# Optimization experiments

Hardware: AMD Instinct MI355X
Metric: run time of the kernel (lower is better)

Reference implementation:

```python
import jax, jax.numpy as jnp
import numpy as np

IN_FEATS = 128
HIDDEN = 32
OUT_CLASSES = 2
N_NODES = 100000
N_EDGES = 625000


def setup_inputs() -> dict:
    key = jax.random.key(0)
    k1, k2, k3, k4, k5, k6, k7 = jax.random.split(key, 7)
    src_nodes = jax.random.randint(k1, (N_EDGES,), 0, N_NODES, dtype=jnp.int64 if jax.config.jax_enable_x64 else jnp.int32)
    dst_nodes = jax.random.randint(k2, (N_EDGES,), 0, N_NODES, dtype=jnp.int64 if jax.config.jax_enable_x64 else jnp.int32)
    node_embed = jax.random.normal(k3, (N_NODES, IN_FEATS), dtype=jnp.float32)
    # Linear params (torch nn.Linear default init: U(-1/sqrt(fan_in), 1/sqrt(fan_in)))
    lim1 = 1.0 / np.sqrt(2 * IN_FEATS)
    W1 = jax.random.uniform(k4, (HIDDEN, 2 * IN_FEATS), jnp.float32, -lim1, lim1)
    b1 = jax.random.uniform(k5, (HIDDEN,), jnp.float32, -lim1, lim1)
    lim2 = 1.0 / np.sqrt(HIDDEN)
    W2 = jax.random.uniform(k6, (OUT_CLASSES, HIDDEN), jnp.float32, -lim2, lim2)
    b2 = jax.random.uniform(k7, (OUT_CLASSES,), jnp.float32, -lim2, lim2)
    return {"src_nodes": src_nodes, "dst_nodes": dst_nodes, "node_embed": node_embed,
            "W1": W1, "b1": b1, "W2": W2, "b2": b2}


def reference(src_nodes, dst_nodes, node_embed, W1, b1, W2, b2):
    # Gather endpoint embeddings: [E, F] each
    src_e = node_embed[src_nodes]
    dst_e = node_embed[dst_nodes]
    # Avoid materializing the concat explicitly in the GEMM by splitting W1:
    # fc1(cat([s, d])) == s @ W1[:, :F].T + d @ W1[:, F:].T + b1
    W1s, W1d = W1[:, :IN_FEATS], W1[:, IN_FEATS:]
    h = jax.nn.relu(src_e @ W1s.T + dst_e @ W1d.T + b1)  # [E, 32]
    logits = h @ W2.T + b2  # [E, out_classes]
    return logits
```

## Files before the change

### kernel.cpp

```cpp
#include <hip/hip_runtime.h>

#define IN_FEATS 128
#define HIDDEN 32

typedef short v8s __attribute__((ext_vector_type(8)));
typedef unsigned short u16x8 __attribute__((ext_vector_type(8)));
typedef float v4f __attribute__((ext_vector_type(4)));

__device__ __forceinline__ unsigned short f2bf(float x) {
    union { float f; unsigned int u; } v; v.f = x;
    const unsigned int r = v.u + 0x7fffu + ((v.u >> 16) & 1u);
    return (unsigned short)(r >> 16);
}
__device__ __forceinline__ float bf2f(unsigned short b) {
    union { float f; unsigned int u; } v; v.u = ((unsigned int)b) << 16;
    return v.f;
}

__global__ __launch_bounds__(256) void pack_W_frags(
    const float* __restrict__ W1,
    unsigned short* __restrict__ Bhi,
    unsigned short* __restrict__ Blo)
{
    const int i = blockIdx.x * 256 + threadIdx.x;
    if (i >= 4 * 4 * 64 * 8) return;
    const int j    = i & 7;
    const int lane = (i >> 3) & 63;
    const int ks   = (i >> 9) & 3;
    const int nb   = i >> 11;
    const int u = nb * 16 + (lane & 15);
    const int k = ks * 32 + ((lane >> 4) & 3) * 8 + j;
    const float w = W1[(u & 31) * (2 * IN_FEATS) + (u >> 5) * IN_FEATS + k];
    const unsigned short hi = f2bf(w);
    Bhi[i] = hi;
    Blo[i] = f2bf(w - bf2f(hi));
}

__global__ __launch_bounds__(256, 4) void precompute_P_mfma(
    const float* __restrict__ embed,
    const unsigned short* __restrict__ Bhi,
    const unsigned short* __restrict__ Blo,
    unsigned short* __restrict__ P,
    int n_nodes)
{
    const int t    = threadIdx.x;
    const int lane = t & 63;
    const int wave = t >> 6;
    const int node0 = blockIdx.x * 64 + wave * 16;
    if (node0 >= n_nodes) return;
    const int last = n_nodes - 1;
    const int row  = min(node0 + (lane & 15), last);
    const int grp  = lane >> 4;

    v8s ahi[4], alo[4];
#pragma unroll
    for (int ks = 0; ks < 4; ++ks) {
        const float* ap = embed + (size_t)row * IN_FEATS + ks * 32 + grp * 8;
        const float4 x0 = *reinterpret_cast<const float4*>(ap);
        const float4 x1 = *reinterpret_cast<const float4*>(ap + 4);
        const float xs[8] = {x0.x, x0.y, x0.z, x0.w, x1.x, x1.y, x1.z, x1.w};
        v8s h, l;
#pragma unroll
        for (int j = 0; j < 8; ++j) {
            const unsigned short hb = f2bf(xs[j]);
            h[j] = (short)hb;
            l[j] = (short)f2bf(xs[j] - bf2f(hb));
        }
        ahi[ks] = h;
        alo[ks] = l;
    }

#pragma unroll
    for (int nb = 0; nb < 4; ++nb) {
        v8s bhi[4], blo[4];
#pragma unroll
        for (int ks = 0; ks < 4; ++ks) {
            const int fi = ((nb * 4 + ks) * 64 + lane) * 8;
            bhi[ks] = *reinterpret_cast<const v8s*>(Bhi + fi);
            blo[ks] = *reinterpret_cast<const v8s*>(Blo + fi);
        }
        v4f acc = {0.f, 0.f, 0.f, 0.f};
#pragma unroll
        for (int ks = 0; ks < 4; ++ks) {
            acc = __builtin_amdgcn_mfma_f32_16x16x32_bf16(ahi[ks], bhi[ks], acc, 0, 0, 0);
            acc = __builtin_amdgcn_mfma_f32_16x16x32_bf16(ahi[ks], blo[ks], acc, 0, 0, 0);
            acc = __builtin_amdgcn_mfma_f32_16x16x32_bf16(alo[ks], bhi[ks], acc, 0, 0, 0);
        }
        const int u = nb * 16 + (lane & 15);
#pragma unroll
        for (int r = 0; r < 4; ++r) {
            const int n = node0 + grp * 4 + r;
            if (n < n_nodes)
                P[(size_t)n * 64 + u] = f2bf(acc[r]);
        }
    }
}

__global__ __launch_bounds__(256) void edge_classify_bf16(
    const int* __restrict__ src,
    const int* __restrict__ dst,
    const unsigned short* __restrict__ P,
    const float* __restrict__ b1,
    const float* __restrict__ W2,
    const float* __restrict__ b2,
    float* __restrict__ out,
    int n_edges)
{
    const int t = threadIdx.x;
    const int e = blockIdx.x * 64 + (t >> 2);
    if (e >= n_edges) return;
    const int q = t & 3;
    const int s = src[e];
    const int d = dst[e];

    const u16x8 ps = *reinterpret_cast<const u16x8*>(P + (size_t)s * 64 + q * 8);
    const u16x8 pd = *reinterpret_cast<const u16x8*>(P + (size_t)d * 64 + 32 + q * 8);

    const float4 b1a = *reinterpret_cast<const float4*>(b1 + q * 8);
    const float4 b1b = *reinterpret_cast<const float4*>(b1 + q * 8 + 4);
    const float4 w0a = *reinterpret_cast<const float4*>(W2 + q * 8);
    const float4 w0b = *reinterpret_cast<const float4*>(W2 + q * 8 + 4);
    const float4 w1a = *reinterpret_cast<const float4*>(W2 + HIDDEN + q * 8);
    const float4 w1b = *reinterpret_cast<const float4*>(W2 + HIDDEN + q * 8 + 4);
    const float bb1[8] = {b1a.x, b1a.y, b1a.z, b1a.w, b1b.x, b1b.y, b1b.z, b1b.w};
    const float ww0[8] = {w0a.x, w0a.y, w0a.z, w0a.w, w0b.x, w0b.y, w0b.z, w0b.w};
    const float ww1[8] = {w1a.x, w1a.y, w1a.z, w1a.w, w1b.x, w1b.y, w1b.z, w1b.w};

    float l0 = 0.f, l1 = 0.f;
#pragma unroll
    for (int j = 0; j < 8; ++j) {
        float h = bf2f(ps[j]) + bf2f(pd[j]) + bb1[j];
        h = fmaxf(h, 0.f);
        l0 = fmaf(h, ww0[j], l0);
        l1 = fmaf(h, ww1[j], l1);
    }
    l0 += __shfl_xor(l0, 1);
    l0 += __shfl_xor(l0, 2);
    l1 += __shfl_xor(l1, 1);
    l1 += __shfl_xor(l1, 2);
    if (q == 0)
        *reinterpret_cast<float2*>(out + (size_t)e * 2) =
            make_float2(l0 + b2[0], l1 + b2[1]);
}

__global__ __launch_bounds__(256) void edge_direct(
    const int* __restrict__ src, const int* __restrict__ dst,
    const float* __restrict__ embed,
    const float* __restrict__ W1, const float* __restrict__ b1,
    const float* __restrict__ W2, const float* __restrict__ b2,
    float* __restrict__ out, int n_edges)
{
    const int e = blockIdx.x * 256 + threadIdx.x;
    if (e >= n_edges) return;
    const int s = src[e], d = dst[e];
    const float* se = embed + (size_t)s * IN_FEATS;
    const float* de = embed + (size_t)d * IN_FEATS;

    float acc[HIDDEN];
#pragma unroll
    for (int hh = 0; hh < HIDDEN; ++hh) acc[hh] = b1[hh];

    for (int c = 0; c < 4; ++c) {
        float es[32], ed[32];
#pragma unroll
        for (int q = 0; q < 8; ++q) {
            const float4 v = *reinterpret_cast<const float4*>(se + c * 32 + q * 4);
            es[q*4+0] = v.x; es[q*4+1] = v.y; es[q*4+2] = v.z; es[q*4+3] = v.w;
            const float4 u = *reinterpret_cast<const float4*>(de + c * 32 + q * 4);
            ed[q*4+0] = u.x; ed[q*4+1] = u.y; ed[q*4+2] = u.z; ed[q*4+3] = u.w;
        }
#pragma unroll
        for (int hh = 0; hh < HIDDEN; ++hh) {
            float acch = acc[hh];
#pragma unroll
            for (int k = 0; k < 32; ++k) {
                acch = fmaf(es[k], W1[hh * 256 + c * 32 + k], acch);
                acch = fmaf(ed[k], W1[hh * 256 + 128 + c * 32 + k], acch);
            }
            acc[hh] = acch;
        }
    }

    float l0 = b2[0], l1 = b2[1];
#pragma unroll
    for (int hh = 0; hh < HIDDEN; ++hh) {
        const float hv = fmaxf(acc[hh], 0.f);
        l0 = fmaf(hv, W2[hh], l0);
        l1 = fmaf(hv, W2[HIDDEN + hh], l1);
    }
    *reinterpret_cast<float2*>(out + (size_t)e * 2) = make_float2(l0, l1);
}

extern "C" void kernel_launch(void* const* d_in, const int* in_sizes, int n_in,
                              void* d_out, int out_size, void* d_ws, size_t ws_size,
                              hipStream_t stream)
{
    const int*   src = (const int*)d_in[0];
    const int*   dst = (const int*)d_in[1];
    const float* emb = (const float*)d_in[2];
    const float* W1  = (const float*)d_in[3];
    const float* b1  = (const float*)d_in[4];
    const float* W2  = (const float*)d_in[5];
    const float* b2  = (const float*)d_in[6];
    float* out = (float*)d_out;

    const int n_edges = in_sizes[0];
    const int n_nodes = in_sizes[2] / IN_FEATS;

    const size_t p_bytes = (size_t)n_nodes * 64 * sizeof(unsigned short);
    const size_t b_elems = 4 * 4 * 64 * 8;
    const size_t need = p_bytes + 2 * b_elems * sizeof(unsigned short);

    if (ws_size >= need && (p_bytes & 15) == 0) {
        unsigned short* P   = (unsigned short*)d_ws;
        unsigned short* Bhi = (unsigned short*)((char*)d_ws + p_bytes);
        unsigned short* Blo = Bhi + b_elems;
        pack_W_frags<<<(int)((b_elems + 255) / 256), 256, 0, stream>>>(W1, Bhi, Blo);
        const int nb_nodes = (n_nodes + 63) / 64;
        precompute_P_mfma<<<nb_nodes, 256, 0, stream>>>(emb, Bhi, Blo, P, n_nodes);
        const int nb_edges4 = (n_edges + 63) / 64;
        edge_classify_bf16<<<nb_edges4, 256, 0, stream>>>(src, dst, P, b1, W2, b2, out, n_edges);
    } else {
        const int nb_edges = (n_edges + 255) / 256;
        edge_direct<<<nb_edges, 256, 0, stream>>>(src, dst, emb, W1, b1, W2, b2, out, n_edges);
    }
}
```

Before: 46.53 us.

## Fuse weight packing, node projection and edge classification into one cooperative kernel

Replaces the three-kernel pipeline (pack W1 fragments, per-node MFMA projection, per-edge gather/classify) with a single persistent cooperative kernel. Each block packs the W1 bf16 hi/lo fragments into shared memory, grid-strides over 16-node tiles to write P, then crosses a grid-wide barrier and grid-strides over edges, two edges per quad per iteration. This is meant to remove two kernel launches and the global round trip of the packed weights, and to add memory-level parallelism in the gather phase. In exchange it adds a grid sync, redundant weight packing in every block, per-call host device-property and occupancy queries, and 32 KB of LDS per block that may limit occupancy.

```diff
diff --git a/kernel.cpp b/kernel.cpp
--- a/kernel.cpp
+++ b/kernel.cpp
@@ -1,4 +1,7 @@
 #include <hip/hip_runtime.h>
+#include <hip/hip_cooperative_groups.h>
+
+namespace cg = cooperative_groups;
 
 #define IN_FEATS 128
 #define HIDDEN 32
@@ -15,6 +18,159 @@
 __device__ __forceinline__ float bf2f(unsigned short b) {
     union { float f; unsigned int u; } v; v.u = ((unsigned int)b) << 16;
     return v.f;
+}
+
+__global__ __launch_bounds__(256, 4) void fused_edge_classifier(
+    const float* __restrict__ embed,
+    const float* __restrict__ W1,
+    const float* __restrict__ b1,
+    const float* __restrict__ W2,
+    const float* __restrict__ b2,
+    const int* __restrict__ src,
+    const int* __restrict__ dst,
+    unsigned short* __restrict__ P,
+    float* __restrict__ out,
+    int n_nodes,
+    int n_edges)
+{
+    __shared__ unsigned short sBhi[8192];
+    __shared__ unsigned short sBlo[8192];
+
+    const int t    = threadIdx.x;
+    const int lane = t & 63;
+    const int wave = t >> 6;
+
+#pragma unroll
+    for (int g0 = 0; g0 < 1024; g0 += 256) {
+        const int g   = g0 + t;
+        const int gl  = g & 63;
+        const int ks  = (g >> 6) & 3;
+        const int nb  = g >> 8;
+        const int u   = nb * 16 + (gl & 15);
+        const int k0  = ks * 32 + ((gl >> 4) & 3) * 8;
+        const float* wp = W1 + (u & 31) * (2 * IN_FEATS) + (u >> 5) * IN_FEATS + k0;
+        const float4 x0 = *reinterpret_cast<const float4*>(wp);
+        const float4 x1 = *reinterpret_cast<const float4*>(wp + 4);
+        const float xs[8] = {x0.x, x0.y, x0.z, x0.w, x1.x, x1.y, x1.z, x1.w};
+        v8s h, l;
+#pragma unroll
+        for (int j = 0; j < 8; ++j) {
+            const unsigned short hb = f2bf(xs[j]);
+            h[j] = (short)hb;
+            l[j] = (short)f2bf(xs[j] - bf2f(hb));
+        }
+        *reinterpret_cast<v8s*>(sBhi + g * 8) = h;
+        *reinterpret_cast<v8s*>(sBlo + g * 8) = l;
+    }
+    __syncthreads();
+
+    const int last = n_nodes - 1;
+    const int grp  = lane >> 4;
+    const int gwid = blockIdx.x * 4 + wave;
+    const int nw   = gridDim.x * 4;
+    const int ntiles = (n_nodes + 15) >> 4;
+
+    for (int tile = gwid; tile < ntiles; tile += nw) {
+        const int node0 = tile << 4;
+        const int row   = min(node0 + (lane & 15), last);
+
+        v8s ahi[4], alo[4];
+#pragma unroll
+        for (int ks = 0; ks < 4; ++ks) {
+            const float* ap = embed + (size_t)row * IN_FEATS + ks * 32 + grp * 8;
+            const float4 x0 = *reinterpret_cast<const float4*>(ap);
+            const float4 x1 = *reinterpret_cast<const float4*>(ap + 4);
+            const float xs[8] = {x0.x, x0.y, x0.z, x0.w, x1.x, x1.y, x1.z, x1.w};
+            v8s h, l;
+#pragma unroll
+            for (int j = 0; j < 8; ++j) {
+                const unsigned short hb = f2bf(xs[j]);
+                h[j] = (short)hb;
+                l[j] = (short)f2bf(xs[j] - bf2f(hb));
+            }
+            ahi[ks] = h;
+            alo[ks] = l;
+        }
+
+#pragma unroll
+        for (int nb = 0; nb < 4; ++nb) {
+            v8s bhi[4], blo[4];
+#pragma unroll
+            for (int ks = 0; ks < 4; ++ks) {
+                const int fi = ((nb * 4 + ks) * 64 + lane) * 8;
+                bhi[ks] = *reinterpret_cast<const v8s*>(sBhi + fi);
+                blo[ks] = *reinterpret_cast<const v8s*>(sBlo + fi);
+            }
+            v4f acc = {0.f, 0.f, 0.f, 0.f};
+#pragma unroll
+            for (int ks = 0; ks < 4; ++ks) {
+                acc = __builtin_amdgcn_mfma_f32_16x16x32_bf16(ahi[ks], bhi[ks], acc, 0, 0, 0);
+                acc = __builtin_amdgcn_mfma_f32_16x16x32_bf16(ahi[ks], blo[ks], acc, 0, 0, 0);
+                acc = __builtin_amdgcn_mfma_f32_16x16x32_bf16(alo[ks], bhi[ks], acc, 0, 0, 0);
+            }
+            const int u = nb * 16 + (lane & 15);
+#pragma unroll
+            for (int r = 0; r < 4; ++r) {
+                const int n = node0 + grp * 4 + r;
+                if (n < n_nodes)
+                    P[(size_t)n * 64 + u] = f2bf(acc[r]);
+            }
+        }
+    }
+
+    cg::this_grid().sync();
+
+    const int q = t & 3;
+    const float4 b1a = *reinterpret_cast<const float4*>(b1 + q * 8);
+    const float4 b1b = *reinterpret_cast<const float4*>(b1 + q * 8 + 4);
+    const float4 w0a = *reinterpret_cast<const float4*>(W2 + q * 8);
+    const float4 w0b = *reinterpret_cast<const float4*>(W2 + q * 8 + 4);
+    const float4 w1a = *reinterpret_cast<const float4*>(W2 + HIDDEN + q * 8);
+    const float4 w1b = *reinterpret_cast<const float4*>(W2 + HIDDEN + q * 8 + 4);
+    const float bb1[8] = {b1a.x, b1a.y, b1a.z, b1a.w, b1b.x, b1b.y, b1b.z, b1b.w};
+    const float ww0[8] = {w0a.x, w0a.y, w0a.z, w0a.w, w0b.x, w0b.y, w0b.z, w0b.w};
+    const float ww1[8] = {w1a.x, w1a.y, w1a.z, w1a.w, w1b.x, w1b.y, w1b.z, w1b.w};
+    const float bias0 = b2[0], bias1 = b2[1];
+
+    const int qid0 = (blockIdx.x * 256 + t) >> 2;
+    const int nq   = gridDim.x * 64;
+
+    for (int e = qid0; e < n_edges; e += 2 * nq) {
+        const int eBr = e + nq;
+        const bool hasB = eBr < n_edges;
+        const int eB = hasB ? eBr : e;
+
+        const int s1 = src[e],  d1 = dst[e];
+        const int s2 = src[eB], d2 = dst[eB];
+        const u16x8 ps1 = *reinterpret_cast<const u16x8*>(P + (size_t)s1 * 64 + q * 8);
+        const u16x8 pd1 = *reinterpret_cast<const u16x8*>(P + (size_t)d1 * 64 + 32 + q * 8);
+        const u16x8 ps2 = *reinterpret_cast<const u16x8*>(P + (size_t)s2 * 64 + q * 8);
+        const u16x8 pd2 = *reinterpret_cast<const u16x8*>(P + (size_t)d2 * 64 + 32 + q * 8);
+
+        float a0 = 0.f, a1 = 0.f, c0 = 0.f, c1 = 0.f;
+#pragma unroll
+        for (int j = 0; j < 8; ++j) {
+            float h1 = bf2f(ps1[j]) + bf2f(pd1[j]) + bb1[j];
+            float h2 = bf2f(ps2[j]) + bf2f(pd2[j]) + bb1[j];
+            h1 = fmaxf(h1, 0.f);
+            h2 = fmaxf(h2, 0.f);
+            a0 = fmaf(h1, ww0[j], a0);
+            a1 = fmaf(h1, ww1[j], a1);
+            c0 = fmaf(h2, ww0[j], c0);
+            c1 = fmaf(h2, ww1[j], c1);
+        }
+        a0 += __shfl_xor(a0, 1); a0 += __shfl_xor(a0, 2);
+        a1 += __shfl_xor(a1, 1); a1 += __shfl_xor(a1, 2);
+        c0 += __shfl_xor(c0, 1); c0 += __shfl_xor(c0, 2);
+        c1 += __shfl_xor(c1, 1); c1 += __shfl_xor(c1, 2);
+        if (q == 0) {
+            *reinterpret_cast<float2*>(out + (size_t)e * 2) =
+                make_float2(a0 + bias0, a1 + bias1);
+            if (hasB)
+                *reinterpret_cast<float2*>(out + (size_t)eBr * 2) =
+                    make_float2(c0 + bias0, c1 + bias1);
+        }
+    }
 }
 
 __global__ __launch_bounds__(256) void pack_W_frags(
@@ -134,10 +290,8 @@
         l0 = fmaf(h, ww0[j], l0);
         l1 = fmaf(h, ww1[j], l1);
     }
-    l0 += __shfl_xor(l0, 1);
-    l0 += __shfl_xor(l0, 2);
-    l1 += __shfl_xor(l1, 1);
-    l1 += __shfl_xor(l1, 2);
+    l0 += __shfl_xor(l0, 1); l0 += __shfl_xor(l0, 2);
+    l1 += __shfl_xor(l1, 1); l1 += __shfl_xor(l1, 2);
     if (q == 0)
         *reinterpret_cast<float2*>(out + (size_t)e * 2) =
             make_float2(l0 + b2[0], l1 + b2[1]);
@@ -209,19 +363,44 @@
 
     const size_t p_bytes = (size_t)n_nodes * 64 * sizeof(unsigned short);
     const size_t b_elems = 4 * 4 * 64 * 8;
-    const size_t need = p_bytes + 2 * b_elems * sizeof(unsigned short);
-
-    if (ws_size >= need && (p_bytes & 15) == 0) {
-        unsigned short* P   = (unsigned short*)d_ws;
-        unsigned short* Bhi = (unsigned short*)((char*)d_ws + p_bytes);
-        unsigned short* Blo = Bhi + b_elems;
-        pack_W_frags<<<(int)((b_elems + 255) / 256), 256, 0, stream>>>(W1, Bhi, Blo);
-        const int nb_nodes = (n_nodes + 63) / 64;
-        precompute_P_mfma<<<nb_nodes, 256, 0, stream>>>(emb, Bhi, Blo, P, n_nodes);
-        const int nb_edges4 = (n_edges + 63) / 64;
-        edge_classify_bf16<<<nb_edges4, 256, 0, stream>>>(src, dst, P, b1, W2, b2, out, n_edges);
-    } else {
+
+    if (ws_size < p_bytes + 2 * b_elems * sizeof(unsigned short)) {
         const int nb_edges = (n_edges + 255) / 256;
         edge_direct<<<nb_edges, 256, 0, stream>>>(src, dst, emb, W1, b1, W2, b2, out, n_edges);
-    }
-}
+        return;
+    }
+
+    unsigned short* P = (unsigned short*)d_ws;
+
+    int dev = 0;
+    (void)hipGetDevice(&dev);
+    hipDeviceProp_t prop;
+    int coop_ok = (hipGetDeviceProperties(&prop, dev) == hipSuccess) &&
+                  prop.cooperativeLaunch;
+    int blocks_per_cu = 0;
+    if (coop_ok) {
+        coop_ok = (hipOccupancyMaxActiveBlocksPerMultiprocessor(
+                       &blocks_per_cu, (const void*)fused_edge_classifier,
+                       256, 0) == hipSuccess) && blocks_per_cu > 0;
+    }
+    if (coop_ok) {
+        const int grid = blocks_per_cu * prop.multiProcessorCount;
+        void* args[] = {
+            (void*)&emb, (void*)&W1, (void*)&b1, (void*)&W2, (void*)&b2,
+            (void*)&src, (void*)&dst, (void*)&P, (void*)&out,
+            (void*)&n_nodes, (void*)&n_edges
+        };
+        if (hipLaunchCooperativeKernel((const void*)fused_edge_classifier,
+                                       dim3(grid), dim3(256), args, 0,
+                                       stream) == hipSuccess)
+            return;
+    }
+
+    unsigned short* Bhi = (unsigned short*)((char*)d_ws + p_bytes);
+    unsigned short* Blo = Bhi + b_elems;
+    pack_W_frags<<<(int)((b_elems + 255) / 256), 256, 0, stream>>>(W1, Bhi, Blo);
+    const int nb_nodes = (n_nodes + 63) / 64;
+    precompute_P_mfma<<<nb_nodes, 256, 0, stream>>>(emb, Bhi, Blo, P, n_nodes);
+    const int nb_edges4 = (n_edges + 63) / 64;
+    edge_classify_bf16<<<nb_edges4, 256, 0, stream>>>(src, dst, P, b1, W2, b2, out, n_edges);
+}
```

Result: slower. 145.0 us (+211.7%).

## Fuse weight packing into precompute via LDS and process two edges per thread

Applied to the files above, without the earlier changes.

Drops the separate pack_W_frags launch. Each precompute block now converts W1 into bf16 hi/lo fragments in shared memory and then handles 128 nodes instead of 64. The edge kernel processes two edges per 4-thread group to add memory-level parallelism and amortize the parameter loads. The aim is to cut one kernel launch plus its global round-trip. The cost is that every block redoes the W1 conversion and uses 32KB of LDS, which can limit occupancy.

```diff
diff --git a/kernel.cpp b/kernel.cpp
--- a/kernel.cpp
+++ b/kernel.cpp
@@ -17,47 +17,30 @@
     return v.f;
 }
 
-__global__ __launch_bounds__(256) void pack_W_frags(
-    const float* __restrict__ W1,
-    unsigned short* __restrict__ Bhi,
-    unsigned short* __restrict__ Blo)
-{
-    const int i = blockIdx.x * 256 + threadIdx.x;
-    if (i >= 4 * 4 * 64 * 8) return;
-    const int j    = i & 7;
-    const int lane = (i >> 3) & 63;
-    const int ks   = (i >> 9) & 3;
-    const int nb   = i >> 11;
-    const int u = nb * 16 + (lane & 15);
-    const int k = ks * 32 + ((lane >> 4) & 3) * 8 + j;
-    const float w = W1[(u & 31) * (2 * IN_FEATS) + (u >> 5) * IN_FEATS + k];
-    const unsigned short hi = f2bf(w);
-    Bhi[i] = hi;
-    Blo[i] = f2bf(w - bf2f(hi));
-}
-
 __global__ __launch_bounds__(256, 4) void precompute_P_mfma(
     const float* __restrict__ embed,
-    const unsigned short* __restrict__ Bhi,
-    const unsigned short* __restrict__ Blo,
+    const float* __restrict__ W1,
     unsigned short* __restrict__ P,
     int n_nodes)
 {
+    __shared__ unsigned short sBhi[8192];
+    __shared__ unsigned short sBlo[8192];
+
     const int t    = threadIdx.x;
     const int lane = t & 63;
     const int wave = t >> 6;
-    const int node0 = blockIdx.x * 64 + wave * 16;
-    if (node0 >= n_nodes) return;
-    const int last = n_nodes - 1;
-    const int row  = min(node0 + (lane & 15), last);
-    const int grp  = lane >> 4;
-
-    v8s ahi[4], alo[4];
-#pragma unroll
-    for (int ks = 0; ks < 4; ++ks) {
-        const float* ap = embed + (size_t)row * IN_FEATS + ks * 32 + grp * 8;
-        const float4 x0 = *reinterpret_cast<const float4*>(ap);
-        const float4 x1 = *reinterpret_cast<const float4*>(ap + 4);
+
+#pragma unroll
+    for (int g0 = 0; g0 < 1024; g0 += 256) {
+        const int g   = g0 + t;
+        const int gl  = g & 63;
+        const int ks  = (g >> 6) & 3;
+        const int nb  = g >> 8;
+        const int u   = nb * 16 + (gl & 15);
+        const int k0  = ks * 32 + ((gl >> 4) & 3) * 8;
+        const float* wp = W1 + (u & 31) * (2 * IN_FEATS) + (u >> 5) * IN_FEATS + k0;
+        const float4 x0 = *reinterpret_cast<const float4*>(wp);
+        const float4 x1 = *reinterpret_cast<const float4*>(wp + 4);
         const float xs[8] = {x0.x, x0.y, x0.z, x0.w, x1.x, x1.y, x1.z, x1.w};
         v8s h, l;
 #pragma unroll
@@ -66,32 +49,61 @@
             h[j] = (short)hb;
             l[j] = (short)f2bf(xs[j] - bf2f(hb));
         }
-        ahi[ks] = h;
-        alo[ks] = l;
-    }
-
-#pragma unroll
-    for (int nb = 0; nb < 4; ++nb) {
-        v8s bhi[4], blo[4];
+        *reinterpret_cast<v8s*>(sBhi + g * 8) = h;
+        *reinterpret_cast<v8s*>(sBlo + g * 8) = l;
+    }
+    __syncthreads();
+
+    const int last = n_nodes - 1;
+    const int grp  = lane >> 4;
+
+#pragma unroll
+    for (int sub = 0; sub < 2; ++sub) {
+        const int node0 = blockIdx.x * 128 + wave * 32 + sub * 16;
+        if (node0 >= n_nodes) break;
+        const int row = min(node0 + (lane & 15), last);
+
+        v8s ahi[4], alo[4];
 #pragma unroll
         for (int ks = 0; ks < 4; ++ks) {
-            const int fi = ((nb * 4 + ks) * 64 + lane) * 8;
-            bhi[ks] = *reinterpret_cast<const v8s*>(Bhi + fi);
-            blo[ks] = *reinterpret_cast<const v8s*>(Blo + fi);
-        }
-        v4f acc = {0.f, 0.f, 0.f, 0.f};
-#pragma unroll
-        for (int ks = 0; ks < 4; ++ks) {
-            acc = __builtin_amdgcn_mfma_f32_16x16x32_bf16(ahi[ks], bhi[ks], acc, 0, 0, 0);
-            acc = __builtin_amdgcn_mfma_f32_16x16x32_bf16(ahi[ks], blo[ks], acc, 0, 0, 0);
-            acc = __builtin_amdgcn_mfma_f32_16x16x32_bf16(alo[ks], bhi[ks], acc, 0, 0, 0);
-        }
-        const int u = nb * 16 + (lane & 15);
-#pragma unroll
-        for (int r = 0; r < 4; ++r) {
-            const int n = node0 + grp * 4 + r;
-            if (n < n_nodes)
-                P[(size_t)n * 64 + u] = f2bf(acc[r]);
+            const float* ap = embed + (size_t)row * IN_FEATS + ks * 32 + grp * 8;
+            const float4 x0 = *reinterpret_cast<const float4*>(ap);
+            const float4 x1 = *reinterpret_cast<const float4*>(ap + 4);
+            const float xs[8] = {x0.x, x0.y, x0.z, x0.w, x1.x, x1.y, x1.z, x1.w};
+            v8s h, l;
+#pragma unroll
+            for (int j = 0; j < 8; ++j) {
+                const unsigned short hb = f2bf(xs[j]);
+                h[j] = (short)hb;
+                l[j] = (short)f2bf(xs[j] - bf2f(hb));
+            }
+            ahi[ks] = h;
+            alo[ks] = l;
+        }
+
+#pragma unroll
+        for (int nb = 0; nb < 4; ++nb) {
+            v8s bhi[4], blo[4];
+#pragma unroll
+            for (int ks = 0; ks < 4; ++ks) {
+                const int fi = ((nb * 4 + ks) * 64 + lane) * 8;
+                bhi[ks] = *reinterpret_cast<const v8s*>(sBhi + fi);
+                blo[ks] = *reinterpret_cast<const v8s*>(sBlo + fi);
+            }
+            v4f acc = {0.f, 0.f, 0.f, 0.f};
+#pragma unroll
+            for (int ks = 0; ks < 4; ++ks) {
+                acc = __builtin_amdgcn_mfma_f32_16x16x32_bf16(ahi[ks], bhi[ks], acc, 0, 0, 0);
+                acc = __builtin_amdgcn_mfma_f32_16x16x32_bf16(ahi[ks], blo[ks], acc, 0, 0, 0);
+                acc = __builtin_amdgcn_mfma_f32_16x16x32_bf16(alo[ks], bhi[ks], acc, 0, 0, 0);
+            }
+            const int u = nb * 16 + (lane & 15);
+#pragma unroll
+            for (int r = 0; r < 4; ++r) {
+                const int n = node0 + grp * 4 + r;
+                if (n < n_nodes)
+                    P[(size_t)n * 64 + u] = f2bf(acc[r]);
+            }
         }
     }
 }
@@ -106,15 +118,21 @@
     float* __restrict__ out,
     int n_edges)
 {
-    const int t = threadIdx.x;
-    const int e = blockIdx.x * 64 + (t >> 2);
-    if (e >= n_edges) return;
-    const int q = t & 3;
-    const int s = src[e];
-    const int d = dst[e];
-
-    const u16x8 ps = *reinterpret_cast<const u16x8*>(P + (size_t)s * 64 + q * 8);
-    const u16x8 pd = *reinterpret_cast<const u16x8*>(P + (size_t)d * 64 + 32 + q * 8);
+    const int t  = threadIdx.x;
+    const int q  = t & 3;
+    const int e0 = blockIdx.x * 128 + (t >> 2);
+    const int e1 = e0 + 64;
+    if (e0 >= n_edges) return;
+    const bool has1 = (e1 < n_edges);
+
+    const int s0 = src[e0], d0 = dst[e0];
+    const int s1 = has1 ? src[e1] : s0;
+    const int d1 = has1 ? dst[e1] : d0;
+
+    const u16x8 ps0 = *reinterpret_cast<const u16x8*>(P + (size_t)s0 * 64 + q * 8);
+    const u16x8 pd0 = *reinterpret_cast<const u16x8*>(P + (size_t)d0 * 64 + 32 + q * 8);
+    const u16x8 ps1 = *reinterpret_cast<const u16x8*>(P + (size_t)s1 * 64 + q * 8);
+    const u16x8 pd1 = *reinterpret_cast<const u16x8*>(P + (size_t)d1 * 64 + 32 + q * 8);
 
     const float4 b1a = *reinterpret_cast<const float4*>(b1 + q * 8);
     const float4 b1b = *reinterpret_cast<const float4*>(b1 + q * 8 + 4);
@@ -126,21 +144,29 @@
     const float ww0[8] = {w0a.x, w0a.y, w0a.z, w0a.w, w0b.x, w0b.y, w0b.z, w0b.w};
     const float ww1[8] = {w1a.x, w1a.y, w1a.z, w1a.w, w1b.x, w1b.y, w1b.z, w1b.w};
 
-    float l0 = 0.f, l1 = 0.f;
+    float a0 = 0.f, a1 = 0.f, c0 = 0.f, c1 = 0.f;
 #pragma unroll
     for (int j = 0; j < 8; ++j) {
-        float h = bf2f(ps[j]) + bf2f(pd[j]) + bb1[j];
-        h = fmaxf(h, 0.f);
-        l0 = fmaf(h, ww0[j], l0);
-        l1 = fmaf(h, ww1[j], l1);
-    }
-    l0 += __shfl_xor(l0, 1);
-    l0 += __shfl_xor(l0, 2);
-    l1 += __shfl_xor(l1, 1);
-    l1 += __shfl_xor(l1, 2);
-    if (q == 0)
-        *reinterpret_cast<float2*>(out + (size_t)e * 2) =
-            make_float2(l0 + b2[0], l1 + b2[1]);
+        float h0 = bf2f(ps0[j]) + bf2f(pd0[j]) + bb1[j];
+        float h1 = bf2f(ps1[j]) + bf2f(pd1[j]) + bb1[j];
+        h0 = fmaxf(h0, 0.f);
+        h1 = fmaxf(h1, 0.f);
+        a0 = fmaf(h0, ww0[j], a0);
+        a1 = fmaf(h0, ww1[j], a1);
+        c0 = fmaf(h1, ww0[j], c0);
+        c1 = fmaf(h1, ww1[j], c1);
+    }
+    a0 += __shfl_xor(a0, 1); a0 += __shfl_xor(a0, 2);
+    a1 += __shfl_xor(a1, 1); a1 += __shfl_xor(a1, 2);
+    c0 += __shfl_xor(c0, 1); c0 += __shfl_xor(c0, 2);
+    c1 += __shfl_xor(c1, 1); c1 += __shfl_xor(c1, 2);
+    if (q == 0) {
+        *reinterpret_cast<float2*>(out + (size_t)e0 * 2) =
+            make_float2(a0 + b2[0], a1 + b2[1]);
+        if (has1)
+            *reinterpret_cast<float2*>(out + (size_t)e1 * 2) =
+                make_float2(c0 + b2[0], c1 + b2[1]);
+    }
 }
 
 __global__ __launch_bounds__(256) void edge_direct(
@@ -208,18 +234,13 @@
     const int n_nodes = in_sizes[2] / IN_FEATS;
 
     const size_t p_bytes = (size_t)n_nodes * 64 * sizeof(unsigned short);
-    const size_t b_elems = 4 * 4 * 64 * 8;
-    const size_t need = p_bytes + 2 * b_elems * sizeof(unsigned short);
-
-    if (ws_size >= need && (p_bytes & 15) == 0) {
-        unsigned short* P   = (unsigned short*)d_ws;
-        unsigned short* Bhi = (unsigned short*)((char*)d_ws + p_bytes);
-        unsigned short* Blo = Bhi + b_elems;
-        pack_W_frags<<<(int)((b_elems + 255) / 256), 256, 0, stream>>>(W1, Bhi, Blo);
-        const int nb_nodes = (n_nodes + 63) / 64;
-        precompute_P_mfma<<<nb_nodes, 256, 0, stream>>>(emb, Bhi, Blo, P, n_nodes);
-        const int nb_edges4 = (n_edges + 63) / 64;
-        edge_classify_bf16<<<nb_edges4, 256, 0, stream>>>(src, dst, P, b1, W2, b2, out, n_edges);
+
+    if (ws_size >= p_bytes) {
+        unsigned short* P = (unsigned short*)d_ws;
+        const int nb_nodes = (n_nodes + 127) / 128;
+        precompute_P_mfma<<<nb_nodes, 256, 0, stream>>>(emb, W1, P, n_nodes);
+        const int nb_edges = (n_edges + 127) / 128;
+        edge_classify_bf16<<<nb_edges, 256, 0, stream>>>(src, dst, P, b1, W2, b2, out, n_edges);
     } else {
         const int nb_edges = (n_edges + 255) / 256;
         edge_direct<<<nb_edges, 256, 0, stream>>>(src, dst, emb, W1, b1, W2, b2, out, n_edges);
```

Result: faster. 41.09 us (-11.7%).
